# Optimization experiments

Measured on AMD Instinct MI355X. Metric: run time of the kernel, lower is better.

Reference implementation:

```python
import jax, jax.numpy as jnp
import numpy as np
from jax import lax

RATIO = 4
NUM_UPS = 2  # log2(RATIO)

def _taps():
    cdf23 = 2.0 * np.array([0.5, 0.305334091185, 0.0, -0.072698593239, 0.0,
                            0.021809577942, 0.0, -0.005192756653, 0.0,
                            0.000807762146, 0.0, -6.0081482e-05])
    base = np.concatenate([cdf23[1:][::-1], cdf23])  # 23 symmetric taps
    return jnp.asarray(base, dtype=jnp.float32)

def _dwconv(x, kern, c):
    # depthwise cross-correlation, matches torch F.conv2d(groups=c)
    return lax.conv_general_dilated(
        x, kern, window_strides=(1, 1), padding='VALID',
        dimension_numbers=('NCHW', 'OIHW', 'NCHW'), feature_group_count=c)

def setup_inputs() -> dict:
    key = jax.random.key(0)
    x = jax.random.normal(key, (16, 8, 160, 160), dtype=jnp.float32)
    return {"x": x}

def reference(x) -> jnp.ndarray:
    taps = _taps()                      # [23]
    pad = (taps.shape[0] - 1) // 2      # 11
    bs, c, h, w = x.shape
    kw = jnp.tile(taps.reshape(1, 1, 1, -1), (c, 1, 1, 1))  # [c,1,1,23]
    kh = jnp.tile(taps.reshape(1, 1, -1, 1), (c, 1, 1, 1))  # [c,1,23,1]
    cur = x
    for k in range(NUM_UPS):
        h, w = h * 2, w * 2
        off = 1 if k == 0 else 0
        up = jnp.zeros((bs, c, h, w), dtype=x.dtype)
        up = up.at[..., off::2, off::2].set(cur)  # zero-insertion upsample
        # width pass: replicate pad + 1x23 depthwise conv
        pw = jnp.pad(up, ((0, 0), (0, 0), (0, 0), (pad, pad)), mode='edge')
        fw = _dwconv(pw, kw, c)
        # height pass: circular pad + 23x1 depthwise conv
        ph = jnp.pad(fw, ((0, 0), (0, 0), (pad, pad), (0, 0)), mode='wrap')
        cur = _dwconv(ph, kh, c)
    return cur
```

## Files before the change

kernel.cpp:

```cpp
#include <hip/hip_runtime.h>

typedef float v4f __attribute__((ext_vector_type(4)));

__device__ constexpr float W12[12] = {
    -1.20162964e-04f,    1.615524292e-03f, -1.0385513306e-02f,  4.3619155884e-02f,
    -1.45397186478e-01f, 6.1066818237e-01f, 6.1066818237e-01f, -1.45397186478e-01f,
     4.3619155884e-02f, -1.0385513306e-02f, 1.615524292e-03f,  -1.20162964e-04f
};

__device__ __forceinline__ int xcd_map(int bid, int nblk) {
    int cpx = nblk >> 3;
    return (bid & 7) * cpx + (bid >> 3);
}

__global__ __launch_bounds__(256) void k_fused(const float* __restrict__ x,
                                               float* __restrict__ out) {
    __shared__ float xw[48][84];
    __shared__ float meb[37][84];
    __shared__ float ew[75][132];

    int bid = xcd_map(blockIdx.x, gridDim.x);
    int ct = bid % 5, rt = (bid / 5) % 5, bc = bid / 25;
    int K0  = rt * 64;
    int MC0 = ct * 64;
    int XB  = K0 / 2 - 8;
    int tid = threadIdx.x;

#pragma unroll
    for (int it = 0; it < 2; ++it) {
        int idx = it * 256 + tid;
        int e = idx / 10, g = idx % 10;
        if (e < 48) {
            int m = XB + e;
            m = m < 0 ? m + 160 : (m >= 160 ? m - 160 : m);
            const float* xr = x + (bc * 160 + m) * 160;
            int qg = 8 * ct - 1 + g;
            int i0 = 4 * qg;
            float flat[20];
#pragma unroll
            for (int b = 0; b < 5; ++b) {
                int bq = qg - 2 + b; bq = bq < 0 ? 0 : (bq > 39 ? 39 : bq);
                *(v4f*)(flat + 4 * b) = *(const v4f*)(xr + 4 * bq);
            }
            float mw[15];
#pragma unroll
            for (int e2 = 0; e2 < 15; ++e2) mw[e2] = flat[e2 + 2];
#pragma unroll
            for (int e2 = 0; e2 < 6; ++e2)  mw[e2] = (i0 - 6 + e2 < 0) ? 0.f : mw[e2];
            float xlast = flat[19];
#pragma unroll
            for (int e2 = 10; e2 < 15; ++e2) mw[e2] = (i0 - 6 + e2 > 159) ? xlast : mw[e2];
            float f[4], cpy[4];
#pragma unroll
            for (int d = 0; d < 4; ++d) {
                float acc = 0.f;
#pragma unroll
                for (int s = 0; s < 12; ++s) acc += W12[s] * mw[d + s];
                f[d] = acc;
                cpy[d] = mw[d + 6];
            }
            if (i0 >= 151) {
#pragma unroll
                for (int d = 0; d < 4; ++d) {
                    int i = i0 + d;
                    float c = 0.f;
#pragma unroll
                    for (int s = 0; s < 12; ++s) if (i + s >= 165) c += W12[s];
                    cpy[d] += c * xlast;
                }
            }
            v4f o0, o1;
            o0.x = f[0]; o0.y = cpy[0]; o0.z = f[1]; o0.w = cpy[1];
            o1.x = f[2]; o1.y = cpy[2]; o1.z = f[3]; o1.w = cpy[3];
            *(v4f*)(&xw[e][8 * g])     = o0;
            *(v4f*)(&xw[e][8 * g + 4]) = o1;
        }
    }
    __syncthreads();

#pragma unroll
    for (int it = 0; it < 3; ++it) {
        int idx = it * 256 + tid;
        int j = idx / 20, lq = idx % 20;
        if (j < 37) {
            v4f acc = {0.f, 0.f, 0.f, 0.f};
#pragma unroll
            for (int s = 0; s < 12; ++s)
                acc += W12[s] * *(const v4f*)(&xw[j + s][4 * lq]);
            *(v4f*)(&meb[j][4 * lq]) = acc;
        }
    }
    __syncthreads();

#pragma unroll
    for (int it = 0; it < 5; ++it) {
        int idx = it * 256 + tid;
        int e = idx / 16, g = idx % 16;
        if (e < 75) {
            const float* row = (e & 1) ? &meb[(e - 1) / 2][0] : &xw[e / 2 + 5][0];
            int i0 = MC0 + 4 * g;
            float flat[20];
#pragma unroll
            for (int b = 0; b < 5; ++b)
                *(v4f*)(flat + 4 * b) = *(const v4f*)(row + 4 * (g + b));
            float mw[15];
#pragma unroll
            for (int e2 = 0; e2 < 15; ++e2) mw[e2] = flat[e2 + 3];
            float m0 = row[8];
#pragma unroll
            for (int e2 = 0; e2 < 5; ++e2)  mw[e2] = (i0 - 5 + e2 < 0) ? m0 : mw[e2];
#pragma unroll
            for (int e2 = 9; e2 < 15; ++e2) mw[e2] = (i0 - 5 + e2 > 319) ? 0.f : mw[e2];
            float f[4], cpy[4];
#pragma unroll
            for (int d = 0; d < 4; ++d) {
                float acc = 0.f;
#pragma unroll
                for (int s = 0; s < 12; ++s) acc += W12[s] * mw[d + s];
                f[d] = acc;
                cpy[d] = mw[d + 5];
            }
            if (i0 <= 5) {
#pragma unroll
                for (int d = 0; d < 4; ++d) {
                    int i = i0 + d;
                    float c = 0.f;
#pragma unroll
                    for (int s = 0; s < 12; ++s) if (i + s <= 5) c += W12[s];
                    cpy[d] += c * m0;
                }
            }
            v4f o0, o1;
            o0.x = cpy[0]; o0.y = f[0]; o0.z = cpy[1]; o0.w = f[1];
            o1.x = cpy[2]; o1.y = f[2]; o1.z = cpy[3]; o1.w = f[3];
            *(v4f*)(&ew[e][8 * g])     = o0;
            *(v4f*)(&ew[e][8 * g + 4]) = o1;
        }
    }
    __syncthreads();

    {
        int c4 = tid & 31, slot = tid >> 5;
        int C0 = MC0 * 2;
        float* base = out + (size_t)bc * 640 * 640 + C0 + 4 * c4;
        v4f w[12];
#pragma unroll
        for (int t = 0; t < 12; ++t) w[t] = *(const v4f*)(&ew[slot * 8 + t][4 * c4]);
#pragma unroll
        for (int u = 0; u < 8; ++u) {
            if (u > 0) {
#pragma unroll
                for (int t = 0; t < 11; ++t) w[t] = w[t + 1];
                w[11] = *(const v4f*)(&ew[slot * 8 + u + 11][4 * c4]);
            }
            int kk = slot * 8 + u;
            __builtin_nontemporal_store(w[5],
                (v4f*)(base + (size_t)(2 * (K0 + kk)) * 640));
            v4f acc = W12[0] * w[0];
#pragma unroll
            for (int s = 1; s < 12; ++s) acc += W12[s] * w[s];
            __builtin_nontemporal_store(acc,
                (v4f*)(base + (size_t)(2 * (K0 + kk) + 1) * 640));
        }
    }
}

extern "C" void kernel_launch(void* const* d_in, const int* in_sizes, int n_in,
                              void* d_out, int out_size, void* d_ws, size_t ws_size,
                              hipStream_t stream) {
    const float* x = (const float*)d_in[0];
    float* out = (float*)d_out;
    k_fused<<<3200, 256, 0, stream>>>(x, out);
}
```

Before: 50.45 us.

## Collapse vertical passes into composed polyphase filters from one LDS stage

Restructures the fused kernel so the two height passes are algebraically composed into polyphase taps (ge/go, 17 taps), precomputed at compile time. Each output row group of four is produced directly from width-filtered input rows in a single shared buffer, so the intermediate meb/ew stages and two barriers go away. The width pass now does both upsampling levels in registers per row. This cuts LDS traffic and synchronisation in exchange for more FMAs per output (17-tap filters) and more register pressure, and edge handling is rewritten, which risks correctness at borders.

```diff
diff --git a/kernel.cpp b/kernel.cpp
--- a/kernel.cpp
+++ b/kernel.cpp
@@ -2,11 +2,25 @@
 
 typedef float v4f __attribute__((ext_vector_type(4)));
 
-__device__ constexpr float W12[12] = {
+constexpr float W12c[12] = {
     -1.20162964e-04f,    1.615524292e-03f, -1.0385513306e-02f,  4.3619155884e-02f,
     -1.45397186478e-01f, 6.1066818237e-01f, 6.1066818237e-01f, -1.45397186478e-01f,
      4.3619155884e-02f, -1.0385513306e-02f, 1.615524292e-03f,  -1.20162964e-04f
 };
+
+struct GTabs { float ge[17]; float go[17]; };
+constexpr GTabs make_gtabs() {
+    GTabs t{};
+    for (int d = 0; d < 17; ++d) { t.ge[d] = 0.f; t.go[d] = 0.f; }
+    for (int v = 0; v < 6; ++v) { t.ge[v + 5] += W12c[2 * v]; t.go[v + 6] += W12c[2 * v + 1]; }
+    for (int v = 0; v < 6; ++v)
+        for (int u = 0; u < 12; ++u) {
+            t.ge[v + u] += W12c[2 * v + 1] * W12c[u];
+            t.go[v + u] += W12c[2 * v]     * W12c[u];
+        }
+    return t;
+}
+__device__ constexpr GTabs G = make_gtabs();
 
 __device__ __forceinline__ int xcd_map(int bid, int nblk) {
     int cpx = nblk >> 3;
@@ -15,152 +29,126 @@
 
 __global__ __launch_bounds__(256) void k_fused(const float* __restrict__ x,
                                                float* __restrict__ out) {
-    __shared__ float xw[48][84];
-    __shared__ float meb[37][84];
-    __shared__ float ew[75][132];
+    __shared__ float ww[48][132];
 
     int bid = xcd_map(blockIdx.x, gridDim.x);
     int ct = bid % 5, rt = (bid / 5) % 5, bc = bid / 25;
-    int K0  = rt * 64;
+    int KQ = rt * 32;
     int MC0 = ct * 64;
-    int XB  = K0 / 2 - 8;
+    int WB = KQ - 8;
     int tid = threadIdx.x;
 
 #pragma unroll
     for (int it = 0; it < 2; ++it) {
         int idx = it * 256 + tid;
-        int e = idx / 10, g = idx % 10;
-        if (e < 48) {
-            int m = XB + e;
-            m = m < 0 ? m + 160 : (m >= 160 ? m - 160 : m);
+        if (idx < 384) {
+            int e = idx >> 3, g = idx & 7;
+            int m = WB + e; m = m < 0 ? m + 160 : (m >= 160 ? m - 160 : m);
             const float* xr = x + (bc * 160 + m) * 160;
-            int qg = 8 * ct - 1 + g;
-            int i0 = 4 * qg;
+            int XC0 = 32 * ct + 4 * g - 8;
+            int qb0 = (32 * ct + 4 * g - 8) >> 2;
             float flat[20];
 #pragma unroll
             for (int b = 0; b < 5; ++b) {
-                int bq = qg - 2 + b; bq = bq < 0 ? 0 : (bq > 39 ? 39 : bq);
+                int bq = qb0 + b; bq = bq < 0 ? 0 : (bq > 39 ? 39 : bq);
                 *(v4f*)(flat + 4 * b) = *(const v4f*)(xr + 4 * bq);
             }
-            float mw[15];
+            if (ct == 0 && g < 2) {
 #pragma unroll
-            for (int e2 = 0; e2 < 15; ++e2) mw[e2] = flat[e2 + 2];
+                for (int p = 0; p < 8; ++p) flat[p] = (XC0 + p < 0) ? 0.f : flat[p];
+            }
+            float x159 = flat[19];
+            if (ct == 4 && g >= 6) {
 #pragma unroll
-            for (int e2 = 0; e2 < 6; ++e2)  mw[e2] = (i0 - 6 + e2 < 0) ? 0.f : mw[e2];
-            float xlast = flat[19];
+                for (int p = 12; p < 20; ++p) flat[p] = (XC0 + p > 159) ? x159 : flat[p];
+            }
+            float mcol[19];
 #pragma unroll
-            for (int e2 = 10; e2 < 15; ++e2) mw[e2] = (i0 - 6 + e2 > 159) ? xlast : mw[e2];
-            float f[4], cpy[4];
-#pragma unroll
-            for (int d = 0; d < 4; ++d) {
+            for (int t = 0; t < 9; ++t) {
                 float acc = 0.f;
 #pragma unroll
-                for (int s = 0; s < 12; ++s) acc += W12[s] * mw[d + s];
-                f[d] = acc;
-                cpy[d] = mw[d + 6];
+                for (int s = 0; s < 12; ++s) acc += W12c[s] * flat[t + s];
+                mcol[2 * t + 1] = acc;
             }
-            if (i0 >= 151) {
 #pragma unroll
-                for (int d = 0; d < 4; ++d) {
-                    int i = i0 + d;
+            for (int t = 0; t < 10; ++t) mcol[2 * t] = flat[5 + t];
+            if (ct == 4 && g >= 5) {
+#pragma unroll
+                for (int t = 0; t < 10; ++t) {
+                    int xi = XC0 + 5 + t;
                     float c = 0.f;
 #pragma unroll
-                    for (int s = 0; s < 12; ++s) if (i + s >= 165) c += W12[s];
-                    cpy[d] += c * xlast;
+                    for (int s = 0; s < 12; ++s) if (xi + s >= 165) c += W12c[s];
+                    mcol[2 * t] += c * x159;
                 }
             }
-            v4f o0, o1;
-            o0.x = f[0]; o0.y = cpy[0]; o0.z = f[1]; o0.w = cpy[1];
-            o1.x = f[2]; o1.y = cpy[2]; o1.z = f[3]; o1.w = cpy[3];
-            *(v4f*)(&xw[e][8 * g])     = o0;
-            *(v4f*)(&xw[e][8 * g + 4]) = o1;
-        }
-    }
-    __syncthreads();
-
+            float mid0 = mcol[5];
+            if (ct == 0 && g == 0) {
 #pragma unroll
-    for (int it = 0; it < 3; ++it) {
-        int idx = it * 256 + tid;
-        int j = idx / 20, lq = idx % 20;
-        if (j < 37) {
-            v4f acc = {0.f, 0.f, 0.f, 0.f};
+                for (int p = 0; p < 5; ++p) mcol[p] = mid0;
+            }
+            if (ct == 4 && g == 7) {
 #pragma unroll
-            for (int s = 0; s < 12; ++s)
-                acc += W12[s] * *(const v4f*)(&xw[j + s][4 * lq]);
-            *(v4f*)(&meb[j][4 * lq]) = acc;
-        }
-    }
-    __syncthreads();
-
+                for (int p = 13; p < 19; ++p) mcol[p] = 0.f;
+            }
+            float oe[8], oo[8];
 #pragma unroll
-    for (int it = 0; it < 5; ++it) {
-        int idx = it * 256 + tid;
-        int e = idx / 16, g = idx % 16;
-        if (e < 75) {
-            const float* row = (e & 1) ? &meb[(e - 1) / 2][0] : &xw[e / 2 + 5][0];
-            int i0 = MC0 + 4 * g;
-            float flat[20];
-#pragma unroll
-            for (int b = 0; b < 5; ++b)
-                *(v4f*)(flat + 4 * b) = *(const v4f*)(row + 4 * (g + b));
-            float mw[15];
-#pragma unroll
-            for (int e2 = 0; e2 < 15; ++e2) mw[e2] = flat[e2 + 3];
-            float m0 = row[8];
-#pragma unroll
-            for (int e2 = 0; e2 < 5; ++e2)  mw[e2] = (i0 - 5 + e2 < 0) ? m0 : mw[e2];
-#pragma unroll
-            for (int e2 = 9; e2 < 15; ++e2) mw[e2] = (i0 - 5 + e2 > 319) ? 0.f : mw[e2];
-            float f[4], cpy[4];
-#pragma unroll
-            for (int d = 0; d < 4; ++d) {
+            for (int d = 0; d < 8; ++d) {
                 float acc = 0.f;
 #pragma unroll
-                for (int s = 0; s < 12; ++s) acc += W12[s] * mw[d + s];
-                f[d] = acc;
-                cpy[d] = mw[d + 5];
+                for (int s = 0; s < 12; ++s) acc += W12c[s] * mcol[d + s];
+                oo[d] = acc;
+                oe[d] = mcol[d + 5];
             }
-            if (i0 <= 5) {
+            if (ct == 0 && g == 0) {
 #pragma unroll
-                for (int d = 0; d < 4; ++d) {
-                    int i = i0 + d;
+                for (int d = 0; d < 6; ++d) {
                     float c = 0.f;
 #pragma unroll
-                    for (int s = 0; s < 12; ++s) if (i + s <= 5) c += W12[s];
-                    cpy[d] += c * m0;
+                    for (int s = 0; s < 12; ++s) if (d + s <= 5) c += W12c[s];
+                    oe[d] += c * mid0;
                 }
             }
-            v4f o0, o1;
-            o0.x = cpy[0]; o0.y = f[0]; o0.z = cpy[1]; o0.w = f[1];
-            o1.x = cpy[2]; o1.y = f[2]; o1.z = cpy[3]; o1.w = f[3];
-            *(v4f*)(&ew[e][8 * g])     = o0;
-            *(v4f*)(&ew[e][8 * g + 4]) = o1;
+#pragma unroll
+            for (int j = 0; j < 4; ++j) {
+                v4f v;
+                v.x = oe[2 * j];     v.y = oo[2 * j];
+                v.z = oe[2 * j + 1]; v.w = oo[2 * j + 1];
+                *(v4f*)(&ww[e][16 * g + 4 * j]) = v;
+            }
         }
     }
     __syncthreads();
 
     {
         int c4 = tid & 31, slot = tid >> 5;
-        int C0 = MC0 * 2;
-        float* base = out + (size_t)bc * 640 * 640 + C0 + 4 * c4;
-        v4f w[12];
+        float* dbase = out + (size_t)bc * 640 * 640 + 2 * MC0 + 4 * c4;
+        int eb = slot * 4;
+        v4f w[17];
 #pragma unroll
-        for (int t = 0; t < 12; ++t) w[t] = *(const v4f*)(&ew[slot * 8 + t][4 * c4]);
+        for (int t = 0; t < 17; ++t) w[t] = *(const v4f*)(&ww[eb + t][4 * c4]);
 #pragma unroll
-        for (int u = 0; u < 8; ++u) {
-            if (u > 0) {
+        for (int q = 0; q < 4; ++q) {
+            if (q > 0) {
 #pragma unroll
-                for (int t = 0; t < 11; ++t) w[t] = w[t + 1];
-                w[11] = *(const v4f*)(&ew[slot * 8 + u + 11][4 * c4]);
+                for (int t = 0; t < 16; ++t) w[t] = w[t + 1];
+                w[16] = *(const v4f*)(&ww[eb + q + 16][4 * c4]);
             }
-            int kk = slot * 8 + u;
-            __builtin_nontemporal_store(w[5],
-                (v4f*)(base + (size_t)(2 * (K0 + kk)) * 640));
-            v4f acc = W12[0] * w[0];
+            int k = KQ + eb + q;
+            float* r0 = dbase + (size_t)(4 * k) * 640;
+            v4f a = W12c[0] * w[2];
 #pragma unroll
-            for (int s = 1; s < 12; ++s) acc += W12[s] * w[s];
-            __builtin_nontemporal_store(acc,
-                (v4f*)(base + (size_t)(2 * (K0 + kk) + 1) * 640));
+            for (int u = 1; u < 12; ++u) a += W12c[u] * w[u + 2];
+            __builtin_nontemporal_store(a, (v4f*)(r0));
+            v4f b = G.ge[0] * w[0];
+#pragma unroll
+            for (int d = 1; d < 17; ++d) b += G.ge[d] * w[d];
+            __builtin_nontemporal_store(b, (v4f*)(r0 + 640));
+            __builtin_nontemporal_store(w[8], (v4f*)(r0 + 1280));
+            v4f c = G.go[0] * w[0];
+#pragma unroll
+            for (int d = 1; d < 17; ++d) c += G.go[d] * w[d];
+            __builtin_nontemporal_store(c, (v4f*)(r0 + 1920));
         }
     }
 }
```

Measured after the change: 45.91 us. -9.0%, faster.
